# Kernel optimization log

Measured on AMD Instinct MI355X. Metric: run time of the kernel, lower is better.

## Reference

```python
import jax, jax.numpy as jnp
import numpy as np
import math

PHI = (1.0 + math.sqrt(5.0)) / 2.0
TWO_PI = 2.0 * math.pi
LUT_SIZE = 4096  # matches get_global_lut(4096, device)

_LUT_SIN = jnp.sin(jnp.arange(LUT_SIZE, dtype=jnp.float32) * (TWO_PI / LUT_SIZE))
_LUT_COS = jnp.cos(jnp.arange(LUT_SIZE, dtype=jnp.float32) * (TWO_PI / LUT_SIZE))


def lut_sin_cos(theta):
    """Linearly-interpolated sin/cos lookup over a 4096-entry table on [0, 2pi)."""
    pos = jnp.mod(theta, TWO_PI) * (LUT_SIZE / TWO_PI)
    i0f = jnp.floor(pos)
    frac = pos - i0f
    i0 = i0f.astype(jnp.int32) % LUT_SIZE
    i1 = (i0 + 1) % LUT_SIZE
    sin_v = _LUT_SIN[i0] * (1.0 - frac) + _LUT_SIN[i1] * frac
    cos_v = _LUT_COS[i0] * (1.0 - frac) + _LUT_COS[i1] * frac
    return sin_v, cos_v


def setup_inputs() -> dict:
    key = jax.random.key(0)
    ks = jax.random.split(key, 6)
    B, D = 8192, 2048
    return {
        "x_real": jax.random.normal(ks[0], (B, D), dtype=jnp.float32),
        "x_imag": jax.random.normal(ks[1], (B, D), dtype=jnp.float32),
        "t": jax.random.uniform(ks[2], (B,), dtype=jnp.float32) * 100.0,
        "w_query": jax.random.normal(ks[3], (D,), dtype=jnp.float32) * 0.02,
        "b_query": jnp.zeros((D,), dtype=jnp.float32),
        "w_osc": jax.random.normal(ks[4], (D,), dtype=jnp.float32) * 0.02,
        "b_osc": jnp.zeros((D,), dtype=jnp.float32),
        "memory_real": jnp.zeros((B, D), dtype=jnp.float32),
        "memory_imag": jnp.zeros((B, D), dtype=jnp.float32),
    }


def reference(x_real, x_imag, t, w_query, b_query, w_osc, b_osc,
              memory_real, memory_imag):
    d_model = x_real.shape[-1]
    scale = math.sqrt(d_model)
    k = 1.0  # default sensitivity

    t_phi = t[:, None] * PHI  # [B, 1]

    # Query phase via LUT
    wl_query = 1.0 + jnp.abs(w_query)
    theta_query = x_real / wl_query + b_query
    sin_q, cos_q = lut_sin_cos(theta_query)  # query_imag, query_real

    # complex_full interference
    interf_real = jnp.sum(cos_q * x_real + sin_q * x_imag, axis=-1)  # [B]
    interf_imag = jnp.sum(cos_q * x_imag - sin_q * x_real, axis=-1)  # [B]
    interference = jnp.sqrt(interf_real ** 2 + interf_imag ** 2)
    interference_norm = jax.nn.sigmoid(interference / scale - 2.0)
    x_inv = 1.0 - interference_norm
    alpha = jnp.exp(-k * x_inv)[:, None]  # [B, 1]

    # Exponential memory blend (memory is detached / constant)
    blended_real = alpha * x_real + (1.0 - alpha) * memory_real
    blended_imag = alpha * x_imag + (1.0 - alpha) * memory_imag

    # Oscillator evolution via second LUT pass
    wl_osc = 1.0 + jnp.abs(w_osc)
    theta_osc_real = blended_real / wl_osc + b_osc + t_phi
    theta_osc_imag = blended_imag / wl_osc + b_osc + t_phi
    sin_or, cos_or = lut_sin_cos(theta_osc_real)
    sin_oi, cos_oi = lut_sin_cos(theta_osc_imag)
    evolved_real = cos_or * cos_oi - sin_or * sin_oi
    evolved_imag = cos_or * sin_oi + sin_or * cos_oi
    return evolved_real, evolved_imag
```

## Files before the change

### kernel.cpp

```cpp
#include <hip/hip_runtime.h>
#include <math.h>


#define PHI_F 1.61803398874989f

typedef float f32x4 __attribute__((ext_vector_type(4)));

__global__ __launch_bounds__(256) void liquid_echo_fused(
    const float* __restrict__ x_real, const float* __restrict__ x_imag,
    const float* __restrict__ t_arr,
    const float* __restrict__ w_query, const float* __restrict__ b_query,
    const float* __restrict__ w_osc,   const float* __restrict__ b_osc,
    const float* __restrict__ mem_r,   const float* __restrict__ mem_i,
    float* __restrict__ out_r, float* __restrict__ out_i,
    float inv_scale)
{
    const int tid = (int)threadIdx.x;
    const int row = (int)blockIdx.x;
    const size_t base4 = (size_t)row << 9;

    const f32x4* xr4 = (const f32x4*)x_real + base4;
    const f32x4* xi4 = (const f32x4*)x_imag + base4;
    const f32x4* wq4 = (const f32x4*)w_query;
    const f32x4* bq4 = (const f32x4*)b_query;
    const f32x4* mr4 = (const f32x4*)mem_r + base4;
    const f32x4* mi4 = (const f32x4*)mem_i + base4;
    const f32x4* wo4 = (const f32x4*)w_osc;
    const f32x4* bo4 = (const f32x4*)b_osc;
    f32x4* or4 = (f32x4*)out_r + base4;
    f32x4* oi4 = (f32x4*)out_i + base4;

    const int c0 = tid;
    const int c1 = tid + 256;

    f32x4 xr0 = __builtin_nontemporal_load(&xr4[c0]);
    f32x4 xr1 = __builtin_nontemporal_load(&xr4[c1]);
    f32x4 xi0 = __builtin_nontemporal_load(&xi4[c0]);
    f32x4 xi1 = __builtin_nontemporal_load(&xi4[c1]);
    f32x4 wq0 = wq4[c0];
    f32x4 wq1 = wq4[c1];
    f32x4 bq0 = bq4[c0];
    f32x4 bq1 = bq4[c1];
    f32x4 mr0 = mr4[c0];
    f32x4 mr1 = mr4[c1];
    f32x4 mi0 = mi4[c0];
    f32x4 mi1 = mi4[c1];
    f32x4 wo0 = wo4[c0];
    f32x4 wo1 = wo4[c1];
    f32x4 bo0 = bo4[c0];
    f32x4 bo1 = bo4[c1];
    const float tv = t_arr[row];

    float accR = 0.f, accI = 0.f;
    #pragma unroll
    for (int j = 0; j < 4; ++j) {
        float xrv = xr0[j];
        float xiv = xi0[j];
        float wl  = 1.f + fabsf(wq0[j]);
        float th  = xrv * __builtin_amdgcn_rcpf(wl) + bq0[j];
        float sq, cq;
        __sincosf(th, &sq, &cq);
        accR = fmaf(cq, xrv, fmaf(sq, xiv, accR));
        accI = fmaf(cq, xiv, fmaf(-sq, xrv, accI));
    }
    #pragma unroll
    for (int j = 0; j < 4; ++j) {
        float xrv = xr1[j];
        float xiv = xi1[j];
        float wl  = 1.f + fabsf(wq1[j]);
        float th  = xrv * __builtin_amdgcn_rcpf(wl) + bq1[j];
        float sq, cq;
        __sincosf(th, &sq, &cq);
        accR = fmaf(cq, xrv, fmaf(sq, xiv, accR));
        accI = fmaf(cq, xiv, fmaf(-sq, xrv, accI));
    }

    #pragma unroll
    for (int off = 32; off > 0; off >>= 1) {
        accR += __shfl_xor(accR, off);
        accI += __shfl_xor(accI, off);
    }
    __shared__ float2 sRI[4];
    const int wave = tid >> 6;
    if ((tid & 63) == 0) sRI[wave] = make_float2(accR, accI);
    asm volatile("s_waitcnt lgkmcnt(0)" ::: "memory");
    __builtin_amdgcn_s_barrier();
    float2 q0 = sRI[0], q1 = sRI[1], q2 = sRI[2], q3 = sRI[3];

    float ir = (q0.x + q1.x) + (q2.x + q3.x);
    float ii = (q0.y + q1.y) + (q2.y + q3.y);
    float interf = sqrtf(fmaf(ir, ir, ii * ii));
    float z     = fmaf(interf, inv_scale, -2.0f);
    float sig   = 1.f / (1.f + __expf(-z));
    float alpha = __expf(sig - 1.f);
    float beta  = 1.f - alpha;
    float tphi2 = 2.0f * PHI_F * tv;

    f32x4 oR, oI;
    #pragma unroll
    for (int j = 0; j < 4; ++j) {
        float br = fmaf(alpha, xr0[j], beta * mr0[j]);
        float bi = fmaf(alpha, xi0[j], beta * mi0[j]);
        float wl = 1.f + fabsf(wo0[j]);
        float ang = fmaf(br + bi, __builtin_amdgcn_rcpf(wl),
                         fmaf(2.f, bo0[j], tphi2));
        float sv, cv;
        __sincosf(ang, &sv, &cv);
        oR[j] = cv;
        oI[j] = sv;
    }
    __builtin_nontemporal_store(oR, &or4[c0]);
    __builtin_nontemporal_store(oI, &oi4[c0]);
    #pragma unroll
    for (int j = 0; j < 4; ++j) {
        float br = fmaf(alpha, xr1[j], beta * mr1[j]);
        float bi = fmaf(alpha, xi1[j], beta * mi1[j]);
        float wl = 1.f + fabsf(wo1[j]);
        float ang = fmaf(br + bi, __builtin_amdgcn_rcpf(wl),
                         fmaf(2.f, bo1[j], tphi2));
        float sv, cv;
        __sincosf(ang, &sv, &cv);
        oR[j] = cv;
        oI[j] = sv;
    }
    __builtin_nontemporal_store(oR, &or4[c1]);
    __builtin_nontemporal_store(oI, &oi4[c1]);
}

__global__ __launch_bounds__(256) void liquid_echo_gen(
    const float* __restrict__ x_real, const float* __restrict__ x_imag,
    const float* __restrict__ t_arr,
    const float* __restrict__ w_query, const float* __restrict__ b_query,
    const float* __restrict__ w_osc,   const float* __restrict__ b_osc,
    const float* __restrict__ mem_r,   const float* __restrict__ mem_i,
    float* __restrict__ out_r, float* __restrict__ out_i,
    int D, float inv_scale)
{
    const int row = blockIdx.x;
    const int d4  = D >> 2;
    const size_t base4 = (size_t)row * d4;

    const float4* xr4 = (const float4*)x_real + base4;
    const float4* xi4 = (const float4*)x_imag + base4;
    const float4* wq4 = (const float4*)w_query;
    const float4* bq4 = (const float4*)b_query;

    float accR = 0.f, accI = 0.f;
    for (int c = (int)threadIdx.x; c < d4; c += 256) {
        float4 xr = xr4[c];
        float4 xi = xi4[c];
        float4 wq = wq4[c];
        float4 bq = bq4[c];
        #pragma unroll
        for (int j = 0; j < 4; ++j) {
            float xrv = (&xr.x)[j];
            float xiv = (&xi.x)[j];
            float wl  = 1.f + fabsf((&wq.x)[j]);
            float th  = xrv * __builtin_amdgcn_rcpf(wl) + (&bq.x)[j];
            float sq, cq;
            __sincosf(th, &sq, &cq);
            accR = fmaf(cq, xrv, fmaf(sq, xiv, accR));
            accI = fmaf(cq, xiv, fmaf(-sq, xrv, accI));
        }
    }
    #pragma unroll
    for (int off = 32; off > 0; off >>= 1) {
        accR += __shfl_xor(accR, off);
        accI += __shfl_xor(accI, off);
    }
    __shared__ float sR[4], sI[4];
    __shared__ float sAlpha;
    const int wave = (int)threadIdx.x >> 6;
    if ((threadIdx.x & 63) == 0) { sR[wave] = accR; sI[wave] = accI; }
    __syncthreads();
    if (threadIdx.x == 0) {
        float ir = sR[0] + sR[1] + sR[2] + sR[3];
        float ii = sI[0] + sI[1] + sI[2] + sI[3];
        float interf = sqrtf(fmaf(ir, ir, ii * ii));
        float z = fmaf(interf, inv_scale, -2.0f);
        float sig = 1.f / (1.f + __expf(-z));
        sAlpha = __expf(sig - 1.f);
    }
    __syncthreads();

    const float alpha = sAlpha;
    const float beta  = 1.f - alpha;
    const float tphi2 = 2.0f * PHI_F * t_arr[row];

    const float4* wo4 = (const float4*)w_osc;
    const float4* bo4 = (const float4*)b_osc;
    const float4* mr4 = (const float4*)mem_r + base4;
    const float4* mi4 = (const float4*)mem_i + base4;
    float4* or4 = (float4*)out_r + base4;
    float4* oi4 = (float4*)out_i + base4;

    for (int c = (int)threadIdx.x; c < d4; c += 256) {
        float4 xr = xr4[c];
        float4 xi = xi4[c];
        float4 wo = wo4[c];
        float4 bo = bo4[c];
        float4 mr = mr4[c];
        float4 mi = mi4[c];
        float4 oR, oI;
        #pragma unroll
        for (int j = 0; j < 4; ++j) {
            float br = fmaf(alpha, (&xr.x)[j], beta * (&mr.x)[j]);
            float bi = fmaf(alpha, (&xi.x)[j], beta * (&mi.x)[j]);
            float wl = 1.f + fabsf((&wo.x)[j]);
            float ang = fmaf(br + bi, __builtin_amdgcn_rcpf(wl),
                             fmaf(2.f, (&bo.x)[j], tphi2));
            float sv, cv;
            __sincosf(ang, &sv, &cv);
            (&oR.x)[j] = cv;
            (&oI.x)[j] = sv;
        }
        or4[c] = oR;
        oi4[c] = oI;
    }
}

extern "C" void kernel_launch(void* const* d_in, const int* in_sizes, int n_in,
                              void* d_out, int out_size, void* d_ws, size_t ws_size,
                              hipStream_t stream) {
    const float* x_real   = (const float*)d_in[0];
    const float* x_imag   = (const float*)d_in[1];
    const float* t_arr    = (const float*)d_in[2];
    const float* w_query  = (const float*)d_in[3];
    const float* b_query  = (const float*)d_in[4];
    const float* w_osc    = (const float*)d_in[5];
    const float* b_osc    = (const float*)d_in[6];
    const float* mem_r    = (const float*)d_in[7];
    const float* mem_i    = (const float*)d_in[8];

    const int B = in_sizes[2];
    const int D = in_sizes[3];

    float* out_r = (float*)d_out;
    float* out_i = out_r + (size_t)B * D;

    const float inv_scale = 1.0f / sqrtf((float)D);

    if ((D >> 2) == 512) {
        liquid_echo_fused<<<B, 256, 0, stream>>>(
            x_real, x_imag, t_arr, w_query, b_query, w_osc, b_osc,
            mem_r, mem_i, out_r, out_i, inv_scale);
    } else {
        liquid_echo_gen<<<B, 256, 0, stream>>>(
            x_real, x_imag, t_arr, w_query, b_query, w_osc, b_osc,
            mem_r, mem_i, out_r, out_i, D, inv_scale);
    }
}
```

Before: 317.9 us.

## Process four rows per block with software-pipelined prefetch of next row

Each block now handles four rows spaced by B/4 instead of one row per block, and issues the x loads for the next row (and the memory loads for the current row) before processing the current one, so global-memory latency overlaps with sincos compute. Per-column reciprocals of the weights and doubled oscillator biases are computed once per block and reused across the four rows. Separate shared-memory slots per row avoid reuse hazards across barriers. Register pressure rises because two rows of x are held at once, which may lower occupancy, and the grid shrinks to B/4 blocks.

```diff
diff --git a/kernel.cpp b/kernel.cpp
--- a/kernel.cpp
+++ b/kernel.cpp
@@ -6,58 +6,43 @@
 
 typedef float f32x4 __attribute__((ext_vector_type(4)));
 
-__global__ __launch_bounds__(256) void liquid_echo_fused(
-    const float* __restrict__ x_real, const float* __restrict__ x_imag,
-    const float* __restrict__ t_arr,
-    const float* __restrict__ w_query, const float* __restrict__ b_query,
-    const float* __restrict__ w_osc,   const float* __restrict__ b_osc,
-    const float* __restrict__ mem_r,   const float* __restrict__ mem_i,
-    float* __restrict__ out_r, float* __restrict__ out_i,
-    float inv_scale)
+struct RowX { f32x4 xr0, xr1, xi0, xi1; };
+struct RowM { f32x4 mr0, mr1, mi0, mi1; };
+struct Params { f32x4 iq0, iq1, bq0, bq1, io0, io1, tb0, tb1; };
+
+__device__ __forceinline__ RowX load_x(const f32x4* __restrict__ xr4,
+                                       const f32x4* __restrict__ xi4,
+                                       size_t base, int c0, int c1) {
+    RowX s;
+    s.xr0 = __builtin_nontemporal_load(&xr4[base + c0]);
+    s.xr1 = __builtin_nontemporal_load(&xr4[base + c1]);
+    s.xi0 = __builtin_nontemporal_load(&xi4[base + c0]);
+    s.xi1 = __builtin_nontemporal_load(&xi4[base + c1]);
+    return s;
+}
+
+__device__ __forceinline__ RowM load_m(const f32x4* __restrict__ mr4,
+                                       const f32x4* __restrict__ mi4,
+                                       size_t base, int c0, int c1) {
+    RowM s;
+    s.mr0 = mr4[base + c0];
+    s.mr1 = mr4[base + c1];
+    s.mi0 = mi4[base + c0];
+    s.mi1 = mi4[base + c1];
+    return s;
+}
+
+__device__ __forceinline__ void process_row(
+    const RowX& x, const RowM& m, float tv, int slot, int tid,
+    const Params& P, float inv_scale,
+    f32x4* __restrict__ or4, f32x4* __restrict__ oi4,
+    size_t base, int c0, int c1, float2 (*sRI)[4])
 {
-    const int tid = (int)threadIdx.x;
-    const int row = (int)blockIdx.x;
-    const size_t base4 = (size_t)row << 9;
-
-    const f32x4* xr4 = (const f32x4*)x_real + base4;
-    const f32x4* xi4 = (const f32x4*)x_imag + base4;
-    const f32x4* wq4 = (const f32x4*)w_query;
-    const f32x4* bq4 = (const f32x4*)b_query;
-    const f32x4* mr4 = (const f32x4*)mem_r + base4;
-    const f32x4* mi4 = (const f32x4*)mem_i + base4;
-    const f32x4* wo4 = (const f32x4*)w_osc;
-    const f32x4* bo4 = (const f32x4*)b_osc;
-    f32x4* or4 = (f32x4*)out_r + base4;
-    f32x4* oi4 = (f32x4*)out_i + base4;
-
-    const int c0 = tid;
-    const int c1 = tid + 256;
-
-    f32x4 xr0 = __builtin_nontemporal_load(&xr4[c0]);
-    f32x4 xr1 = __builtin_nontemporal_load(&xr4[c1]);
-    f32x4 xi0 = __builtin_nontemporal_load(&xi4[c0]);
-    f32x4 xi1 = __builtin_nontemporal_load(&xi4[c1]);
-    f32x4 wq0 = wq4[c0];
-    f32x4 wq1 = wq4[c1];
-    f32x4 bq0 = bq4[c0];
-    f32x4 bq1 = bq4[c1];
-    f32x4 mr0 = mr4[c0];
-    f32x4 mr1 = mr4[c1];
-    f32x4 mi0 = mi4[c0];
-    f32x4 mi1 = mi4[c1];
-    f32x4 wo0 = wo4[c0];
-    f32x4 wo1 = wo4[c1];
-    f32x4 bo0 = bo4[c0];
-    f32x4 bo1 = bo4[c1];
-    const float tv = t_arr[row];
-
     float accR = 0.f, accI = 0.f;
     #pragma unroll
     for (int j = 0; j < 4; ++j) {
-        float xrv = xr0[j];
-        float xiv = xi0[j];
-        float wl  = 1.f + fabsf(wq0[j]);
-        float th  = xrv * __builtin_amdgcn_rcpf(wl) + bq0[j];
+        float xrv = x.xr0[j], xiv = x.xi0[j];
+        float th  = fmaf(xrv, P.iq0[j], P.bq0[j]);
         float sq, cq;
         __sincosf(th, &sq, &cq);
         accR = fmaf(cq, xrv, fmaf(sq, xiv, accR));
@@ -65,27 +50,24 @@
     }
     #pragma unroll
     for (int j = 0; j < 4; ++j) {
-        float xrv = xr1[j];
-        float xiv = xi1[j];
-        float wl  = 1.f + fabsf(wq1[j]);
-        float th  = xrv * __builtin_amdgcn_rcpf(wl) + bq1[j];
+        float xrv = x.xr1[j], xiv = x.xi1[j];
+        float th  = fmaf(xrv, P.iq1[j], P.bq1[j]);
         float sq, cq;
         __sincosf(th, &sq, &cq);
         accR = fmaf(cq, xrv, fmaf(sq, xiv, accR));
         accI = fmaf(cq, xiv, fmaf(-sq, xrv, accI));
     }
-
     #pragma unroll
     for (int off = 32; off > 0; off >>= 1) {
         accR += __shfl_xor(accR, off);
         accI += __shfl_xor(accI, off);
     }
-    __shared__ float2 sRI[4];
     const int wave = tid >> 6;
-    if ((tid & 63) == 0) sRI[wave] = make_float2(accR, accI);
+    if ((tid & 63) == 0) sRI[slot][wave] = make_float2(accR, accI);
     asm volatile("s_waitcnt lgkmcnt(0)" ::: "memory");
     __builtin_amdgcn_s_barrier();
-    float2 q0 = sRI[0], q1 = sRI[1], q2 = sRI[2], q3 = sRI[3];
+    __builtin_amdgcn_sched_barrier(0);
+    float2 q0 = sRI[slot][0], q1 = sRI[slot][1], q2 = sRI[slot][2], q3 = sRI[slot][3];
 
     float ir = (q0.x + q1.x) + (q2.x + q3.x);
     float ii = (q0.y + q1.y) + (q2.y + q3.y);
@@ -99,32 +81,99 @@
     f32x4 oR, oI;
     #pragma unroll
     for (int j = 0; j < 4; ++j) {
-        float br = fmaf(alpha, xr0[j], beta * mr0[j]);
-        float bi = fmaf(alpha, xi0[j], beta * mi0[j]);
-        float wl = 1.f + fabsf(wo0[j]);
-        float ang = fmaf(br + bi, __builtin_amdgcn_rcpf(wl),
-                         fmaf(2.f, bo0[j], tphi2));
+        float br = fmaf(alpha, x.xr0[j], beta * m.mr0[j]);
+        float bi = fmaf(alpha, x.xi0[j], beta * m.mi0[j]);
+        float ang = fmaf(br + bi, P.io0[j], P.tb0[j] + tphi2);
         float sv, cv;
         __sincosf(ang, &sv, &cv);
         oR[j] = cv;
         oI[j] = sv;
     }
-    __builtin_nontemporal_store(oR, &or4[c0]);
-    __builtin_nontemporal_store(oI, &oi4[c0]);
-    #pragma unroll
-    for (int j = 0; j < 4; ++j) {
-        float br = fmaf(alpha, xr1[j], beta * mr1[j]);
-        float bi = fmaf(alpha, xi1[j], beta * mi1[j]);
-        float wl = 1.f + fabsf(wo1[j]);
-        float ang = fmaf(br + bi, __builtin_amdgcn_rcpf(wl),
-                         fmaf(2.f, bo1[j], tphi2));
+    __builtin_nontemporal_store(oR, &or4[base + c0]);
+    __builtin_nontemporal_store(oI, &oi4[base + c0]);
+    #pragma unroll
+    for (int j = 0; j < 4; ++j) {
+        float br = fmaf(alpha, x.xr1[j], beta * m.mr1[j]);
+        float bi = fmaf(alpha, x.xi1[j], beta * m.mi1[j]);
+        float ang = fmaf(br + bi, P.io1[j], P.tb1[j] + tphi2);
         float sv, cv;
         __sincosf(ang, &sv, &cv);
         oR[j] = cv;
         oI[j] = sv;
     }
-    __builtin_nontemporal_store(oR, &or4[c1]);
-    __builtin_nontemporal_store(oI, &oi4[c1]);
+    __builtin_nontemporal_store(oR, &or4[base + c1]);
+    __builtin_nontemporal_store(oI, &oi4[base + c1]);
+}
+
+__global__ __launch_bounds__(256) void liquid_echo_persist(
+    const float* __restrict__ x_real, const float* __restrict__ x_imag,
+    const float* __restrict__ t_arr,
+    const float* __restrict__ w_query, const float* __restrict__ b_query,
+    const float* __restrict__ w_osc,   const float* __restrict__ b_osc,
+    const float* __restrict__ mem_r,   const float* __restrict__ mem_i,
+    float* __restrict__ out_r, float* __restrict__ out_i,
+    int rstride, float inv_scale)
+{
+    const int tid = (int)threadIdx.x;
+    const int c0 = tid, c1 = tid + 256;
+
+    const f32x4* xr4 = (const f32x4*)x_real;
+    const f32x4* xi4 = (const f32x4*)x_imag;
+    const f32x4* mr4 = (const f32x4*)mem_r;
+    const f32x4* mi4 = (const f32x4*)mem_i;
+    const f32x4* wq4 = (const f32x4*)w_query;
+    const f32x4* bq4 = (const f32x4*)b_query;
+    const f32x4* wo4 = (const f32x4*)w_osc;
+    const f32x4* bo4 = (const f32x4*)b_osc;
+    f32x4* or4 = (f32x4*)out_r;
+    f32x4* oi4 = (f32x4*)out_i;
+
+    __shared__ float2 sRI[4][4];
+
+    const int r0 = (int)blockIdx.x;
+    const int r1 = r0 + rstride, r2 = r1 + rstride, r3 = r2 + rstride;
+    const size_t b0 = (size_t)r0 << 9, b1 = (size_t)r1 << 9;
+    const size_t b2 = (size_t)r2 << 9, b3 = (size_t)r3 << 9;
+
+    f32x4 wq0 = wq4[c0], wq1 = wq4[c1], bqa = bq4[c0], bqb = bq4[c1];
+    f32x4 wo0 = wo4[c0], wo1 = wo4[c1], boa = bo4[c0], bob = bo4[c1];
+    Params P;
+    #pragma unroll
+    for (int j = 0; j < 4; ++j) {
+        P.iq0[j] = __builtin_amdgcn_rcpf(1.f + fabsf(wq0[j]));
+        P.iq1[j] = __builtin_amdgcn_rcpf(1.f + fabsf(wq1[j]));
+        P.io0[j] = __builtin_amdgcn_rcpf(1.f + fabsf(wo0[j]));
+        P.io1[j] = __builtin_amdgcn_rcpf(1.f + fabsf(wo1[j]));
+        P.bq0[j] = bqa[j];
+        P.bq1[j] = bqb[j];
+        P.tb0[j] = 2.f * boa[j];
+        P.tb1[j] = 2.f * bob[j];
+    }
+
+    RowX xa = load_x(xr4, xi4, b0, c0, c1);
+    float t0 = t_arr[r0];
+
+    RowM m0 = load_m(mr4, mi4, b0, c0, c1);
+    RowX xb = load_x(xr4, xi4, b1, c0, c1);
+    float t1 = t_arr[r1];
+    __builtin_amdgcn_sched_barrier(0);
+    process_row(xa, m0, t0, 0, tid, P, inv_scale, or4, oi4, b0, c0, c1, sRI);
+
+    RowM m1 = load_m(mr4, mi4, b1, c0, c1);
+    RowX xc = load_x(xr4, xi4, b2, c0, c1);
+    float t2 = t_arr[r2];
+    __builtin_amdgcn_sched_barrier(0);
+    process_row(xb, m1, t1, 1, tid, P, inv_scale, or4, oi4, b1, c0, c1, sRI);
+
+    RowM m2 = load_m(mr4, mi4, b2, c0, c1);
+    RowX xd = load_x(xr4, xi4, b3, c0, c1);
+    float t3 = t_arr[r3];
+    __builtin_amdgcn_sched_barrier(0);
+    process_row(xc, m2, t2, 2, tid, P, inv_scale, or4, oi4, b2, c0, c1, sRI);
+
+    RowM m3 = load_m(mr4, mi4, b3, c0, c1);
+    __builtin_amdgcn_sched_barrier(0);
+    process_row(xd, m3, t3, 3, tid, P, inv_scale, or4, oi4, b3, c0, c1, sRI);
 }
 
 __global__ __launch_bounds__(256) void liquid_echo_gen(
@@ -240,10 +289,11 @@
 
     const float inv_scale = 1.0f / sqrtf((float)D);
 
-    if ((D >> 2) == 512) {
-        liquid_echo_fused<<<B, 256, 0, stream>>>(
+    if (D == 2048 && (B & 3) == 0 && B >= 4) {
+        const int rstride = B >> 2;
+        liquid_echo_persist<<<rstride, 256, 0, stream>>>(
             x_real, x_imag, t_arr, w_query, b_query, w_osc, b_osc,
-            mem_r, mem_i, out_r, out_i, inv_scale);
+            mem_r, mem_i, out_r, out_i, rstride, inv_scale);
     } else {
         liquid_echo_gen<<<B, 256, 0, stream>>>(
             x_real, x_imag, t_arr, w_query, b_query, w_osc, b_osc,
```

New measurement: 319.5 us. No clear change (+0.5%).
